# Kernel tuning notes

Hardware: AMD Instinct MI355X
Metric: run time of the kernel (lower is better)

Reference implementation:

```python
import jax, jax.numpy as jnp
import numpy as np

EMBED_DIM = 1024
NUM_HEADS = 16
HEAD_DIM = EMBED_DIM // NUM_HEADS
B, S = 2, 2048


def setup_inputs() -> dict:
    key = jax.random.key(0)
    ks = jax.random.split(key, 11)
    init = 0.02
    return {
        "query": jax.random.normal(ks[0], (B, S, EMBED_DIM), jnp.float32),
        "key": jax.random.normal(ks[1], (B, S, EMBED_DIM), jnp.float32),
        "value": jax.random.normal(ks[2], (B, S, EMBED_DIM), jnp.float32),
        "Wq": jax.random.normal(ks[3], (EMBED_DIM, EMBED_DIM), jnp.float32) * init,
        "bq": jnp.zeros((EMBED_DIM,), jnp.float32),
        "Wk": jax.random.normal(ks[4], (EMBED_DIM, EMBED_DIM), jnp.float32) * init,
        "bk": jnp.zeros((EMBED_DIM,), jnp.float32),
        "Wv": jax.random.normal(ks[5], (EMBED_DIM, EMBED_DIM), jnp.float32) * init,
        "bv": jnp.zeros((EMBED_DIM,), jnp.float32),
        "Wo": jax.random.normal(ks[6], (EMBED_DIM, EMBED_DIM), jnp.float32) * init,
        "bo": jnp.zeros((EMBED_DIM,), jnp.float32),
    }


def reference(query, key, value, Wq, bq, Wk, bk, Wv, bv, Wo, bo):
    scale = jnp.sqrt(jnp.asarray(HEAD_DIM, query.dtype))
    # projections (torch Linear: x @ W.T + b)
    Q = query @ Wq.T + bq
    K = key @ Wk.T + bk
    V = value @ Wv.T + bv
    # [B, S, E] -> [B, H, S, D]
    def split_heads(x):
        return x.reshape(B, -1, NUM_HEADS, HEAD_DIM).transpose(0, 2, 1, 3)
    Qh, Kh, Vh = split_heads(Q), split_heads(K), split_heads(V)
    # scores: [B, H, S, S] -- the O(N^2) intermediate
    scores = jnp.einsum("bhqd,bhkd->bhqk", Qh, Kh) / scale
    attn_weights = jax.nn.softmax(scores, axis=-1)
    # dropout = 0.0 (eval mode)
    out = jnp.einsum("bhqk,bhkd->bhqd", attn_weights, Vh)
    out = out.transpose(0, 2, 1, 3).reshape(B, -1, EMBED_DIM)
    output = out @ Wo.T + bo
    return output, attn_weights
```

## Files before the change

kernel.cpp:

```cpp
#include <hip/hip_runtime.h>
#include <hip/hip_bf16.h>

typedef unsigned short u16;
typedef u16 u16x8 __attribute__((ext_vector_type(8)));
typedef u16 u16x4 __attribute__((ext_vector_type(4)));
typedef __bf16 bf16x8 __attribute__((ext_vector_type(8)));
typedef float f32x4 __attribute__((ext_vector_type(4)));

#define B_ 2
#define S_ 2048
#define E_ 1024
#define H_ 16
#define D_ 64
#define QSCALE 0.18033688011112042f

__device__ __forceinline__ u16 f2bf(float f) {
    return __builtin_bit_cast(u16, static_cast<__bf16>(f));
}
__device__ __forceinline__ float bf2f(unsigned u) {
    return __builtin_bit_cast(float, u << 16);
}

__device__ __forceinline__ void glds16(const u16* g, u16* l) {
    __builtin_amdgcn_global_load_lds(
        (const __attribute__((address_space(1))) unsigned int*)g,
        (__attribute__((address_space(3))) unsigned int*)l, 16, 0, 0);
}

#define VMCNT0 asm volatile("s_waitcnt vmcnt(0)" ::: "memory")
#define RAW_BAR() do { __builtin_amdgcn_s_barrier(); asm volatile("" ::: "memory"); } while (0)

__device__ __forceinline__ bf16x8 lds_read8(const u16* base, int row, int k) {
    const char* p = (const char*)base + (((row * 128) + (k * 2)) ^ ((row & 7) << 4));
    return __builtin_bit_cast(bf16x8, *(const u16x8*)p);
}

__device__ __forceinline__ f32x4 mfma16x16(bf16x8 a, bf16x8 b, f32x4 c) {
    return __builtin_amdgcn_mfma_f32_16x16x32_bf16(a, b, c, 0, 0, 0);
}

__global__ __launch_bounds__(256) void cvt_kernel(const float* __restrict__ q,
                                                  const float* __restrict__ k,
                                                  const float* __restrict__ v,
                                                  const float* __restrict__ wq,
                                                  const float* __restrict__ wk,
                                                  const float* __restrict__ wv,
                                                  const float* __restrict__ wo,
                                                  u16* __restrict__ qkv_dst,
                                                  u16* __restrict__ w_dst) {
    const int bid = blockIdx.x;
    const float* src;
    u16* dst;
    if (bid < 6144) {
        const int t = bid >> 11, lb = bid & 2047;
        src = (t == 0 ? q : t == 1 ? k : v) + (size_t)lb * 2048;
        dst = qkv_dst + (size_t)t * 4194304 + (size_t)lb * 2048;
    } else {
        const int t = (bid - 6144) >> 9, lb = (bid - 6144) & 511;
        src = (t == 0 ? wq : t == 1 ? wk : t == 2 ? wv : wo) + (size_t)lb * 2048;
        dst = w_dst + (size_t)t * 1048576 + (size_t)lb * 2048;
    }
    const int off = threadIdx.x * 8;
    f32x4 a = *(const f32x4*)(src + off);
    f32x4 b = *(const f32x4*)(src + off + 4);
    u16x8 o;
#pragma unroll
    for (int i = 0; i < 4; ++i) { o[i] = f2bf(a[i]); o[4 + i] = f2bf(b[i]); }
    *(u16x8*)(dst + off) = o;
}

__global__ __launch_bounds__(256) void gemm_qkv(const u16* __restrict__ qkv_bf,
                                                const u16* __restrict__ w_bf,
                                                const float* __restrict__ bq,
                                                const float* __restrict__ bk,
                                                const float* __restrict__ bv,
                                                u16* __restrict__ outbase) {
    const int z = blockIdx.z;
    const u16* A = qkv_bf + (size_t)z * 4194304;
    const u16* W = w_bf + (size_t)z * 1048576;
    const float* bias = (z == 0) ? bq : (z == 1) ? bk : bv;
    u16* outp = outbase + (size_t)z * 4194304;

    const int n0 = blockIdx.x * 128;
    const int m0 = blockIdx.y * 128;
    const int tid = threadIdx.x;
    const int lane = tid & 63, g = lane >> 4, c = lane & 15;
    const int w = tid >> 6, wm = w >> 1, wn = w & 1;

    __shared__ u16 lA[2][8192];
    __shared__ u16 lB[2][8192];

    auto stage = [&](int buf, int kt) {
#pragma unroll
        for (int i = 0; i < 4; ++i) {
            const int chunk = (w * 4 + i) * 64 + lane;
            const int r = chunk >> 3, sg = chunk & 7, ss = sg ^ (r & 7);
            glds16(A + (size_t)(m0 + r) * 1024 + kt * 64 + ss * 8, &lA[buf][(w * 4 + i) * 512]);
            glds16(W + (size_t)(n0 + r) * 1024 + kt * 64 + ss * 8, &lB[buf][(w * 4 + i) * 512]);
        }
    };

    f32x4 acc[4][4] = {};
    stage(0, 0);
    VMCNT0;
    __syncthreads();

    for (int kt = 0; kt < 16; ++kt) {
        const int buf = kt & 1;
        if (kt < 15) stage(buf ^ 1, kt + 1);
#pragma unroll
        for (int ks = 0; ks < 2; ++ks) {
            bf16x8 af[4], bfr[4];
#pragma unroll
            for (int fm = 0; fm < 4; ++fm) af[fm] = lds_read8(lA[buf], wm * 64 + fm * 16 + c, g * 8 + ks * 32);
#pragma unroll
            for (int fn = 0; fn < 4; ++fn) bfr[fn] = lds_read8(lB[buf], wn * 64 + fn * 16 + c, g * 8 + ks * 32);
#pragma unroll
            for (int fm = 0; fm < 4; ++fm)
#pragma unroll
                for (int fn = 0; fn < 4; ++fn)
                    acc[fm][fn] = mfma16x16(af[fm], bfr[fn], acc[fm][fn]);
        }
        VMCNT0;
        RAW_BAR();
    }

    float bv_[4];
#pragma unroll
    for (int fn = 0; fn < 4; ++fn) bv_[fn] = bias[n0 + wn * 64 + fn * 16 + c];

#pragma unroll
    for (int fm = 0; fm < 4; ++fm) {
#pragma unroll
        for (int fn = 0; fn < 4; ++fn) {
            const int mbase = m0 + wm * 64 + fm * 16 + g * 4;
            const int n = n0 + wn * 64 + fn * 16 + c;
            if (z == 2) {
                u16x4 vv;
#pragma unroll
                for (int r = 0; r < 4; ++r) vv[r] = f2bf(acc[fm][fn][r] + bv_[fn]);
                const int b = mbase >> 11, s = mbase & 2047, h = n >> 6, d = n & 63;
                u16* dst = outp + ((size_t)((b * 16 + h) * 64 + d)) * 2048 + s;
                *(u16x4*)dst = vv;
            } else {
                const float sc = (z == 0) ? QSCALE : 1.0f;
#pragma unroll
                for (int r = 0; r < 4; ++r) {
                    const float val = (acc[fm][fn][r] + bv_[fn]) * sc;
                    const int m = mbase + r;
                    const int b = m >> 11, s = m & 2047, h = n >> 6, d = n & 63;
                    outp[((size_t)((b * 16 + h) * 2048 + s)) * 64 + d] = f2bf(val);
                }
            }
        }
    }
}

__global__ __launch_bounds__(256) void gemm_out(const u16* __restrict__ A,
                                                const u16* __restrict__ W,
                                                const float* __restrict__ bias,
                                                float* __restrict__ outp) {
    const int n0 = blockIdx.x * 128;
    const int m0 = blockIdx.y * 128;
    const int tid = threadIdx.x;
    const int lane = tid & 63, g = lane >> 4, c = lane & 15;
    const int w = tid >> 6, wm = w >> 1, wn = w & 1;

    __shared__ u16 lA[2][8192];
    __shared__ u16 lB[2][8192];

    auto stage = [&](int buf, int kt) {
#pragma unroll
        for (int i = 0; i < 4; ++i) {
            const int chunk = (w * 4 + i) * 64 + lane;
            const int r = chunk >> 3, sg = chunk & 7, ss = sg ^ (r & 7);
            glds16(A + (size_t)(m0 + r) * 1024 + kt * 64 + ss * 8, &lA[buf][(w * 4 + i) * 512]);
            glds16(W + (size_t)(n0 + r) * 1024 + kt * 64 + ss * 8, &lB[buf][(w * 4 + i) * 512]);
        }
    };

    f32x4 acc[4][4] = {};
    stage(0, 0);
    VMCNT0;
    __syncthreads();

    for (int kt = 0; kt < 16; ++kt) {
        const int buf = kt & 1;
        if (kt < 15) stage(buf ^ 1, kt + 1);
#pragma unroll
        for (int ks = 0; ks < 2; ++ks) {
            bf16x8 af[4], bfr[4];
#pragma unroll
            for (int fm = 0; fm < 4; ++fm) af[fm] = lds_read8(lA[buf], wm * 64 + fm * 16 + c, g * 8 + ks * 32);
#pragma unroll
            for (int fn = 0; fn < 4; ++fn) bfr[fn] = lds_read8(lB[buf], wn * 64 + fn * 16 + c, g * 8 + ks * 32);
#pragma unroll
            for (int fm = 0; fm < 4; ++fm)
#pragma unroll
                for (int fn = 0; fn < 4; ++fn)
                    acc[fm][fn] = mfma16x16(af[fm], bfr[fn], acc[fm][fn]);
        }
        VMCNT0;
        RAW_BAR();
    }

    float bv_[4];
#pragma unroll
    for (int fn = 0; fn < 4; ++fn) bv_[fn] = bias[n0 + wn * 64 + fn * 16 + c];

#pragma unroll
    for (int fm = 0; fm < 4; ++fm)
#pragma unroll
        for (int fn = 0; fn < 4; ++fn) {
            const int mbase = m0 + wm * 64 + fm * 16 + g * 4;
            const int n = n0 + wn * 64 + fn * 16 + c;
#pragma unroll
            for (int r = 0; r < 4; ++r)
                outp[(size_t)(mbase + r) * 1024 + n] = acc[fm][fn][r] + bv_[fn];
        }
}

__global__ __launch_bounds__(256) void attn_kernel(const u16* __restrict__ Qh,
                                                   const u16* __restrict__ Kh,
                                                   const u16* __restrict__ Vt,
                                                   float* __restrict__ attnW,
                                                   u16* __restrict__ Obf) {
    const int bid = blockIdx.x;
    const int sw = ((bid & 7) << 6) + (bid >> 3);
    const int bh = sw >> 4, qt = sw & 15;
    const int tid = threadIdx.x;
    const int lane = tid & 63, g = lane >> 4, c = lane & 15;
    const int w = tid >> 6;

    __shared__ u16 lQ[8192];
    __shared__ u16 lKV[2][8192];
    __shared__ u16 lP[4][2048];

    const u16* Qbase = Qh + ((size_t)bh * S_ + qt * 128) * D_;
    const u16* Kbase = Kh + (size_t)bh * S_ * D_;
    const u16* Vbase = Vt + (size_t)bh * D_ * S_;

#pragma unroll
    for (int i = 0; i < 4; ++i) {
        const int chunk = (w * 4 + i) * 64 + lane;
        const int r = chunk >> 3, sg = chunk & 7, ss = sg ^ (r & 7);
        glds16(Qbase + r * 64 + ss * 8, &lQ[(w * 4 + i) * 512]);
    }
    auto stageK128 = [&](int buf, int kt2) {
#pragma unroll
        for (int i = 0; i < 4; ++i) {
            const int chunk = (w * 4 + i) * 64 + lane;
            const int r = chunk >> 3, sg = chunk & 7, ss = sg ^ (r & 7);
            glds16(Kbase + (size_t)(kt2 * 128 + r) * 64 + ss * 8, &lKV[buf][(w * 4 + i) * 512]);
        }
    };
    auto stageKV64 = [&](int buf, int kt) {
#pragma unroll
        for (int i = 0; i < 2; ++i) {
            const int chunk = (w * 2 + i) * 64 + lane;
            const int r = chunk >> 3, sg = chunk & 7, ss = sg ^ (r & 7);
            glds16(Kbase + (size_t)(kt * 64 + r) * 64 + ss * 8, &lKV[buf][(w * 2 + i) * 512]);
            glds16(Vbase + (size_t)r * S_ + kt * 64 + ss * 8, &lKV[buf][4096 + (w * 2 + i) * 512]);
        }
    };

    stageK128(0, 0);
    VMCNT0;
    __syncthreads();

    float l_run[2] = {0.f, 0.f};

    for (int kt2 = 0; kt2 < 16; ++kt2) {
        const int buf = kt2 & 1;
        if (kt2 < 15) stageK128(buf ^ 1, kt2 + 1);

#pragma unroll
        for (int sub = 0; sub < 2; ++sub) {
            f32x4 s[4][2] = {};
            __builtin_amdgcn_s_setprio(1);
#pragma unroll
            for (int ks = 0; ks < 2; ++ks) {
                bf16x8 a[4], b[2];
#pragma unroll
                for (int kf = 0; kf < 4; ++kf)
                    a[kf] = lds_read8(lKV[buf], sub * 64 + kf * 16 + c, g * 8 + ks * 32);
#pragma unroll
                for (int qf = 0; qf < 2; ++qf)
                    b[qf] = lds_read8(lQ, w * 32 + qf * 16 + c, g * 8 + ks * 32);
#pragma unroll
                for (int kf = 0; kf < 4; ++kf)
#pragma unroll
                    for (int qf = 0; qf < 2; ++qf)
                        s[kf][qf] = mfma16x16(a[kf], b[qf], s[kf][qf]);
            }
            __builtin_amdgcn_s_setprio(0);
#pragma unroll
            for (int qf = 0; qf < 2; ++qf) {
                float ts = 0.f;
#pragma unroll
                for (int kf = 0; kf < 4; ++kf)
#pragma unroll
                    for (int r = 0; r < 4; ++r) ts += exp2f(s[kf][qf][r]);
                ts += __shfl_xor(ts, 16);
                ts += __shfl_xor(ts, 32);
                l_run[qf] += ts;
            }
        }
        VMCNT0;
        RAW_BAR();
    }
    const float linv[2] = {1.f / l_run[0], 1.f / l_run[1]};

    f32x4 o[2][4] = {};
    stageKV64(0, 0);
    VMCNT0;
    RAW_BAR();

    for (int kt = 0; kt < 32; ++kt) {
        const int buf = kt & 1;
        if (kt < 31) stageKV64(buf ^ 1, kt + 1);

        f32x4 s[4][2] = {};
        __builtin_amdgcn_s_setprio(1);
#pragma unroll
        for (int ks = 0; ks < 2; ++ks) {
            bf16x8 a[4], b[2];
#pragma unroll
            for (int kf = 0; kf < 4; ++kf)
                a[kf] = lds_read8(lKV[buf], kf * 16 + c, g * 8 + ks * 32);
#pragma unroll
            for (int qf = 0; qf < 2; ++qf)
                b[qf] = lds_read8(lQ, w * 32 + qf * 16 + c, g * 8 + ks * 32);
#pragma unroll
            for (int kf = 0; kf < 4; ++kf)
#pragma unroll
                for (int qf = 0; qf < 2; ++qf)
                    s[kf][qf] = mfma16x16(a[kf], b[qf], s[kf][qf]);
        }
        __builtin_amdgcn_s_setprio(0);

        u16* myP = lP[w];
#pragma unroll
        for (int qf = 0; qf < 2; ++qf) {
#pragma unroll
            for (int kf = 0; kf < 4; ++kf) {
                f32x4 p4;
#pragma unroll
                for (int r = 0; r < 4; ++r) p4[r] = exp2f(s[kf][qf][r]) * linv[qf];
#pragma unroll
                for (int rp = 0; rp < 2; ++rp) {
                    const unsigned pk = (unsigned)f2bf(p4[2 * rp]) |
                                        ((unsigned)f2bf(p4[2 * rp + 1]) << 16);
                    const int row = qf * 16 + c;
                    const int col = kf * 16 + g * 4 + 2 * rp;
                    *(unsigned*)((char*)myP + (((row * 128) + (col * 2)) ^ ((row & 7) << 4))) = pk;
                }
            }
        }

        {
            const size_t qbase = (size_t)bh * S_ + (size_t)(qt * 128 + w * 32);
#pragma unroll
            for (int j = 0; j < 8; ++j) {
                const int row = j * 4 + g;
                const unsigned long long pv8 = *(const unsigned long long*)(
                    (const char*)myP + (((row * 128) + c * 8) ^ ((row & 7) << 4)));
                f32x4 o4;
                o4[0] = bf2f((unsigned)(pv8 & 0xffffu));
                o4[1] = bf2f((unsigned)((pv8 >> 16) & 0xffffu));
                o4[2] = bf2f((unsigned)((pv8 >> 32) & 0xffffu));
                o4[3] = bf2f((unsigned)((pv8 >> 48) & 0xffffu));
                __builtin_nontemporal_store(
                    o4, (f32x4*)(attnW + (qbase + row) * S_ + kt * 64 + c * 4));
            }
        }

        __builtin_amdgcn_s_setprio(1);
#pragma unroll
        for (int ks = 0; ks < 2; ++ks) {
            bf16x8 pa[2], vb[4];
#pragma unroll
            for (int fm = 0; fm < 2; ++fm) pa[fm] = lds_read8(myP, fm * 16 + c, g * 8 + ks * 32);
#pragma unroll
            for (int fn = 0; fn < 4; ++fn) vb[fn] = lds_read8(lKV[buf] + 4096, fn * 16 + c, g * 8 + ks * 32);
#pragma unroll
            for (int fm = 0; fm < 2; ++fm)
#pragma unroll
                for (int fn = 0; fn < 4; ++fn)
                    o[fm][fn] = mfma16x16(pa[fm], vb[fn], o[fm][fn]);
        }
        __builtin_amdgcn_s_setprio(0);

        asm volatile("s_waitcnt vmcnt(8)" ::: "memory");
        RAW_BAR();
    }

    const int b2 = bh >> 4, h = bh & 15;
#pragma unroll
    for (int fm = 0; fm < 2; ++fm)
#pragma unroll
        for (int fn = 0; fn < 4; ++fn)
#pragma unroll
            for (int r = 0; r < 4; ++r) {
                const int q = qt * 128 + w * 32 + fm * 16 + g * 4 + r;
                const int d = fn * 16 + c;
                __builtin_nontemporal_store(
                    f2bf(o[fm][fn][r]),
                    &Obf[((size_t)(b2 * S_ + q)) * E_ + h * 64 + d]);
            }
}

extern "C" void kernel_launch(void* const* d_in, const int* in_sizes, int n_in,
                              void* d_out, int out_size, void* d_ws, size_t ws_size,
                              hipStream_t stream) {
    const float* query = (const float*)d_in[0];
    const float* key_ = (const float*)d_in[1];
    const float* value = (const float*)d_in[2];
    const float* Wq = (const float*)d_in[3];
    const float* bq = (const float*)d_in[4];
    const float* Wk = (const float*)d_in[5];
    const float* bk = (const float*)d_in[6];
    const float* Wv = (const float*)d_in[7];
    const float* bv = (const float*)d_in[8];
    const float* Wo = (const float*)d_in[9];
    const float* bo = (const float*)d_in[10];

    u16* qkv_bf = (u16*)d_ws;
    u16* w_bf = qkv_bf + (size_t)12 * 1024 * 1024;
    u16* Qh = qkv_bf + (size_t)16 * 1024 * 1024;
    u16* Obf = qkv_bf;

    float* out0 = (float*)d_out;
    float* attnW = out0 + (size_t)B_ * S_ * E_;

    cvt_kernel<<<8192, 256, 0, stream>>>(query, key_, value, Wq, Wk, Wv, Wo, qkv_bf, w_bf);

    gemm_qkv<<<dim3(8, 32, 3), 256, 0, stream>>>(qkv_bf, w_bf, bq, bk, bv, Qh);

    attn_kernel<<<512, 256, 0, stream>>>(Qh, Qh + (size_t)4 * 1024 * 1024,
                                         Qh + (size_t)8 * 1024 * 1024, attnW, Obf);

    gemm_out<<<dim3(8, 32), 256, 0, stream>>>(Obf, w_bf + (size_t)3 * 1024 * 1024, bo, (float*)d_out);
}
```

Measured before the change: 237.1 us.

## Split attention row-sum pass into separate kernel with smaller query tiles

Moves the first pass of the two-pass attention (computing softmax denominators via QK^T and exp-sum) into its own kernel that uses 64-row query tiles, keeps Q in registers, and launches 1024 blocks. The second kernel reads precomputed inverse row sums from workspace and only does the normalized P write and PV. This is meant to raise parallelism and cut LDS/register pressure in the sum pass. In exchange it adds a kernel launch and a workspace round trip, and K is re-streamed by twice as many blocks.

Measured after the change: 266.2 us. 12.3% more time.

```diff
diff --git a/kernel.cpp b/kernel.cpp
--- a/kernel.cpp
+++ b/kernel.cpp
@@ -220,11 +220,84 @@
         }
 }
 
-__global__ __launch_bounds__(256) void attn_kernel(const u16* __restrict__ Qh,
-                                                   const u16* __restrict__ Kh,
-                                                   const u16* __restrict__ Vt,
-                                                   float* __restrict__ attnW,
-                                                   u16* __restrict__ Obf) {
+__global__ __launch_bounds__(256) void attn_sums(const u16* __restrict__ Qh,
+                                                 const u16* __restrict__ Kh,
+                                                 float* __restrict__ linv_ws) {
+    const int bid = blockIdx.x;
+    const int sw = ((bid & 7) << 7) + (bid >> 3);
+    const int bh = sw >> 5, qt = sw & 31;
+    const int tid = threadIdx.x;
+    const int lane = tid & 63, g = lane >> 4, c = lane & 15;
+    const int w = tid >> 6;
+
+    __shared__ u16 lK[2][8192];
+
+    const u16* Qbase = Qh + ((size_t)bh * S_ + qt * 64) * D_;
+    const u16* Kbase = Kh + (size_t)bh * S_ * D_;
+
+    bf16x8 qreg[2];
+#pragma unroll
+    for (int ks = 0; ks < 2; ++ks)
+        qreg[ks] = __builtin_bit_cast(bf16x8,
+            *(const u16x8*)(Qbase + (size_t)(w * 16 + c) * 64 + ks * 32 + g * 8));
+
+    auto stageK128 = [&](int buf, int kt2) {
+#pragma unroll
+        for (int i = 0; i < 4; ++i) {
+            const int chunk = (w * 4 + i) * 64 + lane;
+            const int r = chunk >> 3, sg = chunk & 7, ss = sg ^ (r & 7);
+            glds16(Kbase + (size_t)(kt2 * 128 + r) * 64 + ss * 8, &lK[buf][(w * 4 + i) * 512]);
+        }
+    };
+
+    stageK128(0, 0);
+    VMCNT0;
+    __syncthreads();
+
+    float l_run = 0.f;
+
+    for (int kt2 = 0; kt2 < 16; ++kt2) {
+        const int buf = kt2 & 1;
+        if (kt2 < 15) stageK128(buf ^ 1, kt2 + 1);
+
+#pragma unroll
+        for (int sub = 0; sub < 2; ++sub) {
+            f32x4 s[4] = {};
+            __builtin_amdgcn_s_setprio(1);
+#pragma unroll
+            for (int ks = 0; ks < 2; ++ks) {
+                bf16x8 a[4];
+#pragma unroll
+                for (int kf = 0; kf < 4; ++kf)
+                    a[kf] = lds_read8(lK[buf], sub * 64 + kf * 16 + c, g * 8 + ks * 32);
+#pragma unroll
+                for (int kf = 0; kf < 4; ++kf)
+                    s[kf] = mfma16x16(a[kf], qreg[ks], s[kf]);
+            }
+            __builtin_amdgcn_s_setprio(0);
+            float ts = 0.f;
+#pragma unroll
+            for (int kf = 0; kf < 4; ++kf)
+#pragma unroll
+                for (int r = 0; r < 4; ++r) ts += exp2f(s[kf][r]);
+            ts += __shfl_xor(ts, 16);
+            ts += __shfl_xor(ts, 32);
+            l_run += ts;
+        }
+        VMCNT0;
+        RAW_BAR();
+    }
+
+    if (lane < 16)
+        linv_ws[(size_t)bh * S_ + qt * 64 + w * 16 + c] = 1.f / l_run;
+}
+
+__global__ __launch_bounds__(256) void attn_pv(const u16* __restrict__ Qh,
+                                               const u16* __restrict__ Kh,
+                                               const u16* __restrict__ Vt,
+                                               const float* __restrict__ linv_ws,
+                                               float* __restrict__ attnW,
+                                               u16* __restrict__ Obf) {
     const int bid = blockIdx.x;
     const int sw = ((bid & 7) << 6) + (bid >> 3);
     const int bh = sw >> 4, qt = sw & 15;
@@ -246,14 +319,6 @@
         const int r = chunk >> 3, sg = chunk & 7, ss = sg ^ (r & 7);
         glds16(Qbase + r * 64 + ss * 8, &lQ[(w * 4 + i) * 512]);
     }
-    auto stageK128 = [&](int buf, int kt2) {
-#pragma unroll
-        for (int i = 0; i < 4; ++i) {
-            const int chunk = (w * 4 + i) * 64 + lane;
-            const int r = chunk >> 3, sg = chunk & 7, ss = sg ^ (r & 7);
-            glds16(Kbase + (size_t)(kt2 * 128 + r) * 64 + ss * 8, &lKV[buf][(w * 4 + i) * 512]);
-        }
-    };
     auto stageKV64 = [&](int buf, int kt) {
 #pragma unroll
         for (int i = 0; i < 2; ++i) {
@@ -264,57 +329,14 @@
         }
     };
 
-    stageK128(0, 0);
-    VMCNT0;
-    __syncthreads();
-
-    float l_run[2] = {0.f, 0.f};
-
-    for (int kt2 = 0; kt2 < 16; ++kt2) {
-        const int buf = kt2 & 1;
-        if (kt2 < 15) stageK128(buf ^ 1, kt2 + 1);
-
-#pragma unroll
-        for (int sub = 0; sub < 2; ++sub) {
-            f32x4 s[4][2] = {};
-            __builtin_amdgcn_s_setprio(1);
-#pragma unroll
-            for (int ks = 0; ks < 2; ++ks) {
-                bf16x8 a[4], b[2];
-#pragma unroll
-                for (int kf = 0; kf < 4; ++kf)
-                    a[kf] = lds_read8(lKV[buf], sub * 64 + kf * 16 + c, g * 8 + ks * 32);
-#pragma unroll
-                for (int qf = 0; qf < 2; ++qf)
-                    b[qf] = lds_read8(lQ, w * 32 + qf * 16 + c, g * 8 + ks * 32);
-#pragma unroll
-                for (int kf = 0; kf < 4; ++kf)
-#pragma unroll
-                    for (int qf = 0; qf < 2; ++qf)
-                        s[kf][qf] = mfma16x16(a[kf], b[qf], s[kf][qf]);
-            }
-            __builtin_amdgcn_s_setprio(0);
-#pragma unroll
-            for (int qf = 0; qf < 2; ++qf) {
-                float ts = 0.f;
-#pragma unroll
-                for (int kf = 0; kf < 4; ++kf)
-#pragma unroll
-                    for (int r = 0; r < 4; ++r) ts += exp2f(s[kf][qf][r]);
-                ts += __shfl_xor(ts, 16);
-                ts += __shfl_xor(ts, 32);
-                l_run[qf] += ts;
-            }
-        }
-        VMCNT0;
-        RAW_BAR();
-    }
-    const float linv[2] = {1.f / l_run[0], 1.f / l_run[1]};
+    const float linv[2] = {
+        linv_ws[(size_t)bh * S_ + qt * 128 + w * 32 + c],
+        linv_ws[(size_t)bh * S_ + qt * 128 + w * 32 + 16 + c]};
 
     f32x4 o[2][4] = {};
     stageKV64(0, 0);
     VMCNT0;
-    RAW_BAR();
+    __syncthreads();
 
     for (int kt = 0; kt < 32; ++kt) {
         const int buf = kt & 1;
@@ -429,6 +451,7 @@
     u16* w_bf = qkv_bf + (size_t)12 * 1024 * 1024;
     u16* Qh = qkv_bf + (size_t)16 * 1024 * 1024;
     u16* Obf = qkv_bf;
+    float* linv_ws = (float*)(qkv_bf + (size_t)8 * 1024 * 1024);
 
     float* out0 = (float*)d_out;
     float* attnW = out0 + (size_t)B_ * S_ * E_;
@@ -437,8 +460,10 @@
 
     gemm_qkv<<<dim3(8, 32, 3), 256, 0, stream>>>(qkv_bf, w_bf, bq, bk, bv, Qh);
 
-    attn_kernel<<<512, 256, 0, stream>>>(Qh, Qh + (size_t)4 * 1024 * 1024,
-                                         Qh + (size_t)8 * 1024 * 1024, attnW, Obf);
+    attn_sums<<<1024, 256, 0, stream>>>(Qh, Qh + (size_t)4 * 1024 * 1024, linv_ws);
+
+    attn_pv<<<512, 256, 0, stream>>>(Qh, Qh + (size_t)4 * 1024 * 1024,
+                                     Qh + (size_t)8 * 1024 * 1024, linv_ws, attnW, Obf);
 
     gemm_out<<<dim3(8, 32), 256, 0, stream>>>(Obf, w_bf + (size_t)3 * 1024 * 1024, bo, (float*)d_out);
 }
```
